# Optimization experiments

Measured on AMD Instinct MI355X. Metric: run time of the kernel, lower is better.

Reference implementation:

```python
import jax, jax.numpy as jnp
import numpy as np

B, S, HID = 2, 2048, 2048
H, KV, D = 16, 4, 128
THETA = 10000.0


def _apply_rope(x):
    # x: [B, h, S, D]; rotate even/odd interleaved halves, concat (original layout)
    seq = x.shape[2]
    pos = jnp.arange(seq, dtype=jnp.float32)
    inv_freq = 1.0 / (THETA ** (jnp.arange(0, D, 2, dtype=jnp.float32) / D))
    freqs = pos[:, None] * inv_freq[None, :]            # [S, D/2]
    cos = jnp.cos(freqs)[None, None]                    # [1,1,S,D/2]
    sin = jnp.sin(freqs)[None, None]
    x1, x2 = x[..., ::2], x[..., 1::2]
    return jnp.concatenate([x1 * cos - x2 * sin, x1 * sin + x2 * cos], axis=-1)


def setup_inputs() -> dict:
    key = jax.random.key(0)
    ks = jax.random.split(key, 5)
    x = jax.random.normal(ks[0], (B, S, HID), jnp.float32)
    Wq = jax.random.normal(ks[1], (HID, H * D), jnp.float32) * 0.02
    Wk = jax.random.normal(ks[2], (HID, KV * D), jnp.float32) * 0.02
    Wv = jax.random.normal(ks[3], (HID, KV * D), jnp.float32) * 0.02
    Wo = jax.random.normal(ks[4], (H * D, HID), jnp.float32) * 0.02
    mask = jnp.tril(jnp.ones((S, S), jnp.int32))[None, None]  # causal [1,1,S,S]
    return {"x": x, "mask": mask, "Wq": Wq, "Wk": Wk, "Wv": Wv, "Wo": Wo}


def reference(x, mask, Wq, Wk, Wv, Wo):
    b, s, _ = x.shape
    q = (x @ Wq).reshape(b, s, H, D).transpose(0, 2, 1, 3)   # [B,H,S,D]
    k = (x @ Wk).reshape(b, s, KV, D).transpose(0, 2, 1, 3)  # [B,KV,S,D]
    v = (x @ Wv).reshape(b, s, KV, D).transpose(0, 2, 1, 3)
    q = _apply_rope(q)
    k = _apply_rope(k)
    rep = H // KV
    k = jnp.repeat(k, rep, axis=1)  # GQA repeat_interleave -> [B,H,S,D]
    v = jnp.repeat(v, rep, axis=1)
    scores = jnp.einsum('bhqd,bhkd->bhqk', q, k) / jnp.sqrt(jnp.float32(D))
    scores = jnp.where(mask == 0, -jnp.inf, scores)
    attn = jax.nn.softmax(scores, axis=-1)  # dropout p=0 -> identity
    out = jnp.einsum('bhqk,bhkd->bhqd', attn, v)
    out = out.transpose(0, 2, 1, 3).reshape(b, s, H * D)
    return out @ Wo
```

## Files before the change

### kernel.cpp

```cpp
#include <hip/hip_runtime.h>
#include <cstdint>


typedef __attribute__((ext_vector_type(8))) short short8;
typedef __attribute__((ext_vector_type(8))) _Float16 half8;
typedef __attribute__((ext_vector_type(2))) __fp16 fp16x2;
typedef __attribute__((ext_vector_type(4))) float f32x4;
typedef __attribute__((ext_vector_type(16))) float f32x16;
typedef unsigned short u16;
typedef unsigned int u32;

#define NLOG_THETA_D2 (-0.14391156831212787f)
#define QSC_L2E 0.12751779437543f
#define M2SHIFT 17.3123404906676f

__device__ __forceinline__ u16 f2bf(float f) {
    u32 u = __float_as_uint(f);
    u += 0x7fffu + ((u >> 16) & 1u);
    return (u16)(u >> 16);
}
__device__ __forceinline__ float bf2f(u16 u) { return __uint_as_float(((u32)u) << 16); }
__device__ __forceinline__ u16 bf2h(u16 b) {
    union { _Float16 h; u16 u; } cv;
    cv.h = (_Float16)bf2f(b);
    return cv.u;
}
__device__ __forceinline__ u16 f2h(float f) {
    union { _Float16 h; u16 u; } cv;
    cv.h = (_Float16)f;
    return cv.u;
}
__device__ __forceinline__ float fast_exp2(float x) { return __builtin_amdgcn_exp2f(x); }

__device__ __forceinline__ void async_copy16(const void* g, void* lds) {
    __builtin_amdgcn_global_load_lds(
        (const __attribute__((address_space(1))) u32*)(uintptr_t)g,
        (__attribute__((address_space(3))) u32*)(uintptr_t)lds, 16, 0, 0);
}

__global__ __launch_bounds__(256)
void prep_kernel(const float* __restrict__ x, const float* __restrict__ Wq,
                 const float* __restrict__ Wk, const float* __restrict__ Wv,
                 u16* __restrict__ xb, u16* __restrict__ Wqkvt) {
    __shared__ float tile[32][33];
    int blk = blockIdx.x;
    if (blk < 8192) {
        int i = blk * 256 + threadIdx.x;
        float4 v = ((const float4*)x)[i];
        ushort4 o;
        o.x = f2bf(v.x); o.y = f2bf(v.y); o.z = f2bf(v.z); o.w = f2bf(v.w);
        ((ushort4*)xb)[i] = o;
        return;
    }
    const float* in; int C, orow, bx, by;
    if (blk < 12288)      { int j = blk - 8192;  in = Wq; C = 2048; orow = 0;    bx = j & 63; by = j >> 6; }
    else if (blk < 13312) { int j = blk - 12288; in = Wk; C = 512;  orow = 2048; bx = j & 15; by = j >> 4; }
    else                  { int j = blk - 13312; in = Wv; C = 512;  orow = 2560; bx = j & 15; by = j >> 4; }
    int r0 = by * 32, c0 = bx * 32;
    int tx = threadIdx.x & 31, ty = threadIdx.x >> 5;
#pragma unroll
    for (int j = 0; j < 4; ++j)
        tile[ty + j * 8][tx] = in[(size_t)(r0 + ty + j * 8) * C + c0 + tx];
    __syncthreads();
#pragma unroll
    for (int j = 0; j < 4; ++j)
        Wqkvt[(size_t)(orow + c0 + ty + j * 8) * 2048 + r0 + tx] = f2bf(tile[tx][ty + j * 8]);
}

__global__ __launch_bounds__(256)
void rope_vt_kernel(const u16* __restrict__ qkv, const float* __restrict__ Wo,
                    u16* __restrict__ qR, u16* __restrict__ kR,
                    u16* __restrict__ vT, u16* __restrict__ Wot) {
    int blk = blockIdx.x;
    if (blk < 4096) {
        int row = blk;
        float pos = (float)(row & 2047);
        const u16* rbase = qkv + (size_t)row * 3072;
        for (int t = threadIdx.x; t < 640; t += 256) {
            ushort4 uv; int c4; u16* ob; float sc;
            if (t < 512) {
                c4 = t * 4; uv = *(const ushort4*)(rbase + c4);
                ob = qR + (size_t)row * 2048 + (c4 & ~127); sc = QSC_L2E;
            } else {
                int u = t - 512; c4 = u * 4; uv = *(const ushort4*)(rbase + 2048 + c4);
                ob = kR + (size_t)row * 512 + (c4 & ~127); sc = 1.0f;
            }
            int j = (c4 & 127) >> 1;
            float x0 = bf2f(uv.x), x1 = bf2f(uv.y), x2 = bf2f(uv.z), x3 = bf2f(uv.w);
            float s1, c1, s2, c2;
            sincosf(pos * __expf(NLOG_THETA_D2 * (float)j), &s1, &c1);
            sincosf(pos * __expf(NLOG_THETA_D2 * (float)(j + 1)), &s2, &c2);
            float o1 = (x0 * c1 - x1 * s1) * sc;
            float o2 = (x2 * c2 - x3 * s2) * sc;
            float o3 = (x0 * s1 + x1 * c1) * sc;
            float o4 = (x2 * s2 + x3 * c2) * sc;
            *(u32*)&ob[j]      = (u32)f2bf(o1) | ((u32)f2bf(o2) << 16);
            *(u32*)&ob[64 + j] = (u32)f2bf(o3) | ((u32)f2bf(o4) << 16);
        }
        return;
    }
    int tx = threadIdx.x & 31, ty = threadIdx.x >> 5;
    if (blk < 6144) {
        __shared__ u16 tile[32][33];
        int j = blk - 4096;
        int b = j >> 10, rem = j & 1023;
        int c0 = (rem & 15) * 32, r0 = (rem >> 4) * 32;
        const u16* in = qkv + (size_t)b * 2048 * 3072 + 2560;
        u16* out = vT + (size_t)b * 512 * 2048;
#pragma unroll
        for (int i = 0; i < 4; ++i)
            tile[ty + i * 8][tx] = in[(size_t)(r0 + ty + i * 8) * 3072 + c0 + tx];
        __syncthreads();
#pragma unroll
        for (int i = 0; i < 4; ++i)
            out[(size_t)(c0 + ty + i * 8) * 2048 + r0 + tx] = bf2h(tile[tx][ty + i * 8]);
        return;
    }
    {
        __shared__ float tile[32][33];
        int j = blk - 6144;
        int c0 = (j & 63) * 32, r0 = (j >> 6) * 32;
#pragma unroll
        for (int i = 0; i < 4; ++i)
            tile[ty + i * 8][tx] = Wo[(size_t)(r0 + ty + i * 8) * 2048 + c0 + tx];
        __syncthreads();
#pragma unroll
        for (int i = 0; i < 4; ++i)
            Wot[(size_t)(c0 + ty + i * 8) * 2048 + r0 + tx] = f2bf(tile[tx][ty + i * 8]);
    }
}

template <int OBF>
__global__ __launch_bounds__(256)
void gemm_bf16(const u16* __restrict__ A, const u16* __restrict__ Bt,
               void* __restrict__ Cout, int M, int N, int K) {
    __shared__ __align__(16) u16 As[128 * 32];
    __shared__ __align__(16) u16 Bs[128 * 32];
    const int tid = threadIdx.x, wid = tid >> 6, lane = tid & 63;
    const int quad = lane >> 4, l16 = lane & 15;
    const int m0 = blockIdx.y * 128, n0 = blockIdx.x * 128;
    const int wm0 = (wid >> 1) * 64, wn0 = (wid & 1) * 64;
    f32x4 acc[4][4] = {};

    for (int k0 = 0; k0 < K; k0 += 32) {
#pragma unroll
        for (int rr = 0; rr < 2; ++rr) {
            int s = rr * 256 + wid * 64 + lane;
            int row = s >> 2;
            int c = (s & 3) ^ ((row >> 1) & 3);
            async_copy16(A + (size_t)(m0 + row) * K + k0 + c * 8,
                         &As[(size_t)(rr * 256 + wid * 64) * 8]);
            async_copy16(Bt + (size_t)(n0 + row) * K + k0 + c * 8,
                         &Bs[(size_t)(rr * 256 + wid * 64) * 8]);
        }
        __syncthreads();
        short8 a[4], b[4];
#pragma unroll
        for (int i = 0; i < 4; ++i) {
            int ra = wm0 + i * 16 + l16;
            a[i] = *(const short8*)&As[ra * 32 + ((quad ^ ((ra >> 1) & 3)) << 3)];
            int rb = wn0 + i * 16 + l16;
            b[i] = *(const short8*)&Bs[rb * 32 + ((quad ^ ((rb >> 1) & 3)) << 3)];
        }
#pragma unroll
        for (int i = 0; i < 4; ++i)
#pragma unroll
            for (int j = 0; j < 4; ++j)
                acc[i][j] = __builtin_amdgcn_mfma_f32_16x16x32_bf16(a[i], b[j], acc[i][j], 0, 0, 0);
        __syncthreads();
    }
#pragma unroll
    for (int i = 0; i < 4; ++i) {
        int rb = m0 + wm0 + i * 16 + quad * 4;
#pragma unroll
        for (int j = 0; j < 4; ++j) {
            int col = n0 + wn0 + j * 16 + l16;
#pragma unroll
            for (int r = 0; r < 4; ++r) {
                if (OBF) ((u16*)Cout)[(size_t)(rb + r) * N + col] = f2bf(acc[i][j][r]);
                else     ((float*)Cout)[(size_t)(rb + r) * N + col] = acc[i][j][r];
            }
        }
    }
}

__global__ __launch_bounds__(256, 2)
void attn_kernel(const u16* __restrict__ qR, const u16* __restrict__ kR,
                 const u16* __restrict__ vT, u16* __restrict__ ao,
                 u16* __restrict__ Opart, float* __restrict__ lpart) {
    __shared__ __align__(16) u16 bufK[2][64 * 128];
    __shared__ __align__(16) u16 bufV[2][128 * 64];
    const int tid = threadIdx.x, wid = tid >> 6, lane = tid & 63;
    const int l31 = lane & 31, h = lane >> 5;
    const int b = blockIdx.z, hh = blockIdx.y;
    const int bx = blockIdx.x;
    int qt, t0, nt, chunk;
    bool split;
    if (bx < 16) {
        qt = 15 - (bx >> 1); chunk = bx & 1; split = true;
        nt = qt + 1; t0 = chunk ? (qt + 1) : 0;
    } else {
        qt = 23 - bx; chunk = 0; split = false;
        nt = 2 * qt + 2; t0 = 0;
    }
    const int kvh = hh >> 2;
    const int q0 = qt * 128;
    const u16* kB = kR + (size_t)b * 2048 * 512 + kvh * 128;
    const u16* vB = vT + (size_t)(b * 512 + kvh * 128) * 2048;

    const u16* kSrc[4]; const u16* vSrc[4]; int ldsOff[4];
#pragma unroll
    for (int rr = 0; rr < 4; ++rr) {
        int s = rr * 256 + wid * 64 + lane;
        int rK = s >> 4, cK = (s & 15) ^ (rK & 7);
        kSrc[rr] = kB + (size_t)(t0 * 64 + rK) * 512 + cK * 8;
        int rV = s >> 3, cV = (s & 7) ^ (rV & 7);
        vSrc[rr] = vB + (size_t)rV * 2048 + t0 * 64 + cV * 8;
        ldsOff[rr] = (rr * 256 + wid * 64) * 8;
    }
    auto stage = [&](int buf) {
#pragma unroll
        for (int rr = 0; rr < 4; ++rr) {
            async_copy16(kSrc[rr], &bufK[buf][ldsOff[rr]]);
            async_copy16(vSrc[rr], &bufV[buf][ldsOff[rr]]);
            kSrc[rr] += 64 * 512;
            vSrc[rr] += 64;
        }
    };

    const int rq = wid * 32 + l31;
    const u16* qrow = qR + (size_t)(b * 2048 + q0 + rq) * 2048 + hh * 128;
    short8 aQ[8];
#pragma unroll
    for (int kd = 0; kd < 8; ++kd)
        aQ[kd] = *(const short8*)(qrow + kd * 16 + h * 8);

    f32x16 oacc[4] = {};
    float lp = 0.f;
    const int qg = q0 + rq;

    stage(0);
    for (int t = 0; t < nt; ++t) {
        const int cur = t & 1;
        __syncthreads();
        if (t + 1 < nt) stage(cur ^ 1);

        f32x16 sacc[2] = {};
#pragma unroll
        for (int kd = 0; kd < 8; ++kd)
#pragma unroll
            for (int mt = 0; mt < 2; ++mt) {
                int rk = mt * 32 + l31;
                short8 aK = *(const short8*)&bufK[cur][rk * 128 + (((kd * 2 + h) ^ (rk & 7)) << 3)];
                sacc[mt] = __builtin_amdgcn_mfma_f32_32x32x16_bf16(aK, aQ[kd], sacc[mt], 0, 0, 0);
            }

        const int tg = t0 + t;
        const int kk0 = tg * 64;
        u32 pk[2][8];
        const bool domask = (tg >= 2 * qt);
        auto softpack = [&](bool dm) {
#pragma unroll
            for (int mt = 0; mt < 2; ++mt) {
                const int kvb = kk0 + mt * 32 + 4 * h;
#pragma unroll
                for (int p = 0; p < 8; ++p) {
                    int r0 = 2 * p;
                    float s0 = sacc[mt][r0], s1 = sacc[mt][r0 + 1];
                    float p0, p1;
                    if (dm) {
                        int kv0 = kvb + (r0 & 3) + 8 * (r0 >> 2);
                        p0 = (kv0 <= qg)     ? fast_exp2(s0 - M2SHIFT) : 0.f;
                        p1 = (kv0 + 1 <= qg) ? fast_exp2(s1 - M2SHIFT) : 0.f;
                    } else {
                        p0 = fast_exp2(s0 - M2SHIFT);
                        p1 = fast_exp2(s1 - M2SHIFT);
                    }
                    lp += p0 + p1;
                    union { fp16x2 h; u32 u; } cv;
                    cv.h = __builtin_amdgcn_cvt_pkrtz(p0, p1);
                    pk[mt][p] = cv.u;
                }
            }
        };
        if (domask) softpack(true); else softpack(false);

#pragma unroll
        for (int ks = 0; ks < 4; ++ks) {
            int mt = ks >> 1, k2 = ks & 1;
            u32 own0 = pk[mt][4 * k2 + 2 * h + 0];
            u32 own1 = pk[mt][4 * k2 + 2 * h + 1];
            u32 snd0 = pk[mt][4 * k2 + 2 * (h ^ 1) + 0];
            u32 snd1 = pk[mt][4 * k2 + 2 * (h ^ 1) + 1];
            u32 rc0 = __shfl_xor((int)snd0, 32, 64);
            u32 rc1 = __shfl_xor((int)snd1, 32, 64);
            union { half8 v; u32 u[4]; } bP;
            bP.u[0] = h ? rc0 : own0;
            bP.u[1] = h ? rc1 : own1;
            bP.u[2] = h ? own0 : rc0;
            bP.u[3] = h ? own1 : rc1;
#pragma unroll
            for (int dt = 0; dt < 4; ++dt) {
                int rv = dt * 32 + l31;
                union { short8 s; half8 v; } aV;
                aV.s = *(const short8*)&bufV[cur][rv * 64 + (((ks * 2 + h) ^ (rv & 7)) << 3)];
                oacc[dt] = __builtin_amdgcn_mfma_f32_32x32x16_f16(aV.v, bP.v, oacc[dt], 0, 0, 0);
            }
        }
    }

    lp += __shfl_xor(lp, 32, 64);

    if (!split) {
        float linv = 1.0f / lp;
        u16* orow = ao + (size_t)(b * 2048 + qg) * 2048 + hh * 128;
#pragma unroll
        for (int dt = 0; dt < 4; ++dt)
#pragma unroll
            for (int g = 0; g < 4; ++g) {
                ushort4 o4;
                o4.x = f2bf(oacc[dt][4 * g + 0] * linv);
                o4.y = f2bf(oacc[dt][4 * g + 1] * linv);
                o4.z = f2bf(oacc[dt][4 * g + 2] * linv);
                o4.w = f2bf(oacc[dt][4 * g + 3] * linv);
                *(ushort4*)&orow[dt * 32 + 8 * g + 4 * h] = o4;
            }
    } else {
        const int gi = ((b * 16 + hh) * 8 + (qt - 8)) * 2 + chunk;
        u16* prow = Opart + ((size_t)gi * 128 + rq) * 128;
#pragma unroll
        for (int dt = 0; dt < 4; ++dt)
#pragma unroll
            for (int g = 0; g < 4; ++g) {
                ushort4 o4;
                o4.x = f2h(oacc[dt][4 * g + 0]);
                o4.y = f2h(oacc[dt][4 * g + 1]);
                o4.z = f2h(oacc[dt][4 * g + 2]);
                o4.w = f2h(oacc[dt][4 * g + 3]);
                *(ushort4*)&prow[dt * 32 + 8 * g + 4 * h] = o4;
            }
        if (h == 0) lpart[gi * 128 + rq] = lp;
    }
}

__global__ __launch_bounds__(256)
void combine_kernel(const u16* __restrict__ Opart, const float* __restrict__ lpart,
                    u16* __restrict__ ao) {
    const int gi = blockIdx.x;
    const int q8 = gi & 7, hh = (gi >> 3) & 15, b = gi >> 7;
    const int r = threadIdx.x >> 1, hf = threadIdx.x & 1;
    const size_t p0 = (((size_t)gi * 2 + 0) * 128 + r) * 128 + hf * 64;
    const size_t p1 = (((size_t)gi * 2 + 1) * 128 + r) * 128 + hf * 64;
    const float l0 = lpart[(gi * 2 + 0) * 128 + r];
    const float l1 = lpart[(gi * 2 + 1) * 128 + r];
    const float inv = 1.0f / (l0 + l1);
    u16* orow = ao + ((size_t)(b * 2048 + (q8 + 8) * 128 + r)) * 2048 + hh * 128 + hf * 64;
#pragma unroll
    for (int c = 0; c < 8; ++c) {
        half8 a = *(const half8*)&Opart[p0 + c * 8];
        half8 d = *(const half8*)&Opart[p1 + c * 8];
        union { ushort4 q[2]; u16 e[8]; } o;
#pragma unroll
        for (int j = 0; j < 8; ++j)
            o.e[j] = f2bf(((float)a[j] + (float)d[j]) * inv);
        *(ushort4*)&orow[c * 8]     = o.q[0];
        *(ushort4*)&orow[c * 8 + 4] = o.q[1];
    }
}

extern "C" void kernel_launch(void* const* d_in, const int* in_sizes, int n_in,
                              void* d_out, int out_size, void* d_ws, size_t ws_size,
                              hipStream_t stream) {
    const float* x  = (const float*)d_in[0];
    const float* Wq = (const float*)d_in[2];
    const float* Wk = (const float*)d_in[3];
    const float* Wv = (const float*)d_in[4];
    const float* Wo = (const float*)d_in[5];
    float* out = (float*)d_out;

    char* ws = (char*)d_ws;
    u16* Wqkvt = (u16*)(ws);
    u16* Wot   = Wqkvt;
    u16* xb_ao = (u16*)(ws + 12582912);
    u16* qkv   = (u16*)(ws + 29360128);
    u16* Opart = (u16*)(ws + 29360128);
    float* lpart = (float*)(ws + 29360128 + 16777216);
    u16* qR    = (u16*)(ws + 54525952);
    u16* kR    = (u16*)(ws + 71303168);
    u16* vT    = (u16*)(ws + 75497472);

    dim3 blk(256);
    prep_kernel<<<14336, blk, 0, stream>>>(x, Wq, Wk, Wv, xb_ao, Wqkvt);
    gemm_bf16<1><<<dim3(24, 32), blk, 0, stream>>>(xb_ao, Wqkvt, qkv, 4096, 3072, 2048);
    rope_vt_kernel<<<10240, blk, 0, stream>>>(qkv, Wo, qR, kR, vT, Wot);
    attn_kernel<<<dim3(24, 16, 2), blk, 0, stream>>>(qR, kR, vT, xb_ao, Opart, lpart);
    combine_kernel<<<256, blk, 0, stream>>>(Opart, lpart, xb_ao);
    gemm_bf16<0><<<dim3(16, 32), blk, 0, stream>>>(xb_ao, Wot, out, 4096, 2048, 2048);
}
```

Before: 388.0 us.

## Load K/V directly from global in attention, drop LDS staging, XCD-aware block mapping

The attention kernel stops staging K and V tiles through double-buffered shared memory with async copies and barriers. Each lane now reads its MFMA operands straight from global memory (relying on L2 for reuse across the four waves and the GQA head group). A 1D grid is remapped so that blocks sharing a batch and KV head land on the same XCD, and launch bounds are raised to allow 4 blocks per CU. This removes LDS traffic and syncs, but every wave now issues redundant global loads with no prefetch overlap, so memory latency may be exposed.

```diff
diff --git a/kernel.cpp b/kernel.cpp
--- a/kernel.cpp
+++ b/kernel.cpp
@@ -184,49 +184,37 @@
     }
 }
 
-__global__ __launch_bounds__(256, 2)
+__global__ __launch_bounds__(256, 4)
 void attn_kernel(const u16* __restrict__ qR, const u16* __restrict__ kR,
                  const u16* __restrict__ vT, u16* __restrict__ ao,
                  u16* __restrict__ Opart, float* __restrict__ lpart) {
-    __shared__ __align__(16) u16 bufK[2][64 * 128];
-    __shared__ __align__(16) u16 bufV[2][128 * 64];
     const int tid = threadIdx.x, wid = tid >> 6, lane = tid & 63;
     const int l31 = lane & 31, h = lane >> 5;
-    const int b = blockIdx.z, hh = blockIdx.y;
-    const int bx = blockIdx.x;
+    const int bid = blockIdx.x;
+    const int xcd = bid & 7;
+    const int b = xcd >> 2, kvh = xcd & 3;
+    const int j = bid >> 3;
+    const int hh = kvh * 4 + (j & 3);
+    const int sched = j >> 2;
     int qt, t0, nt, chunk;
     bool split;
-    if (bx < 16) {
-        qt = 15 - (bx >> 1); chunk = bx & 1; split = true;
+    if (sched < 16) {
+        qt = 15 - (sched >> 1); chunk = sched & 1; split = true;
         nt = qt + 1; t0 = chunk ? (qt + 1) : 0;
     } else {
-        qt = 23 - bx; chunk = 0; split = false;
+        qt = 23 - sched; chunk = 0; split = false;
         nt = 2 * qt + 2; t0 = 0;
     }
-    const int kvh = hh >> 2;
     const int q0 = qt * 128;
     const u16* kB = kR + (size_t)b * 2048 * 512 + kvh * 128;
     const u16* vB = vT + (size_t)(b * 512 + kvh * 128) * 2048;
 
-    const u16* kSrc[4]; const u16* vSrc[4]; int ldsOff[4];
-#pragma unroll
-    for (int rr = 0; rr < 4; ++rr) {
-        int s = rr * 256 + wid * 64 + lane;
-        int rK = s >> 4, cK = (s & 15) ^ (rK & 7);
-        kSrc[rr] = kB + (size_t)(t0 * 64 + rK) * 512 + cK * 8;
-        int rV = s >> 3, cV = (s & 7) ^ (rV & 7);
-        vSrc[rr] = vB + (size_t)rV * 2048 + t0 * 64 + cV * 8;
-        ldsOff[rr] = (rr * 256 + wid * 64) * 8;
-    }
-    auto stage = [&](int buf) {
-#pragma unroll
-        for (int rr = 0; rr < 4; ++rr) {
-            async_copy16(kSrc[rr], &bufK[buf][ldsOff[rr]]);
-            async_copy16(vSrc[rr], &bufV[buf][ldsOff[rr]]);
-            kSrc[rr] += 64 * 512;
-            vSrc[rr] += 64;
-        }
-    };
+    const u16* kP0 = kB + (size_t)(t0 * 64 + l31) * 512 + h * 8;
+    const u16* kP1 = kP0 + (size_t)32 * 512;
+    const u16* vP0 = vB + (size_t)l31 * 2048 + t0 * 64 + h * 8;
+    const u16* vP1 = vP0 + (size_t)32 * 2048;
+    const u16* vP2 = vP0 + (size_t)64 * 2048;
+    const u16* vP3 = vP0 + (size_t)96 * 2048;
 
     const int rq = wid * 32 + l31;
     const u16* qrow = qR + (size_t)(b * 2048 + q0 + rq) * 2048 + hh * 128;
@@ -239,21 +227,16 @@
     float lp = 0.f;
     const int qg = q0 + rq;
 
-    stage(0);
     for (int t = 0; t < nt; ++t) {
-        const int cur = t & 1;
-        __syncthreads();
-        if (t + 1 < nt) stage(cur ^ 1);
-
         f32x16 sacc[2] = {};
 #pragma unroll
-        for (int kd = 0; kd < 8; ++kd)
-#pragma unroll
-            for (int mt = 0; mt < 2; ++mt) {
-                int rk = mt * 32 + l31;
-                short8 aK = *(const short8*)&bufK[cur][rk * 128 + (((kd * 2 + h) ^ (rk & 7)) << 3)];
-                sacc[mt] = __builtin_amdgcn_mfma_f32_32x32x16_bf16(aK, aQ[kd], sacc[mt], 0, 0, 0);
-            }
+        for (int kd = 0; kd < 8; ++kd) {
+            sacc[0] = __builtin_amdgcn_mfma_f32_32x32x16_bf16(
+                *(const short8*)(kP0 + kd * 16), aQ[kd], sacc[0], 0, 0, 0);
+            sacc[1] = __builtin_amdgcn_mfma_f32_32x32x16_bf16(
+                *(const short8*)(kP1 + kd * 16), aQ[kd], sacc[1], 0, 0, 0);
+        }
+        kP0 += 64 * 512; kP1 += 64 * 512;
 
         const int tg = t0 + t;
         const int kk0 = tg * 64;
@@ -299,14 +282,17 @@
             bP.u[1] = h ? rc1 : own1;
             bP.u[2] = h ? own0 : rc0;
             bP.u[3] = h ? own1 : rc1;
-#pragma unroll
-            for (int dt = 0; dt < 4; ++dt) {
-                int rv = dt * 32 + l31;
-                union { short8 s; half8 v; } aV;
-                aV.s = *(const short8*)&bufV[cur][rv * 64 + (((ks * 2 + h) ^ (rv & 7)) << 3)];
-                oacc[dt] = __builtin_amdgcn_mfma_f32_32x32x16_f16(aV.v, bP.v, oacc[dt], 0, 0, 0);
-            }
-        }
+            union { short8 s; half8 v; } aV0, aV1, aV2, aV3;
+            aV0.s = *(const short8*)(vP0 + ks * 16);
+            aV1.s = *(const short8*)(vP1 + ks * 16);
+            aV2.s = *(const short8*)(vP2 + ks * 16);
+            aV3.s = *(const short8*)(vP3 + ks * 16);
+            oacc[0] = __builtin_amdgcn_mfma_f32_32x32x16_f16(aV0.v, bP.v, oacc[0], 0, 0, 0);
+            oacc[1] = __builtin_amdgcn_mfma_f32_32x32x16_f16(aV1.v, bP.v, oacc[1], 0, 0, 0);
+            oacc[2] = __builtin_amdgcn_mfma_f32_32x32x16_f16(aV2.v, bP.v, oacc[2], 0, 0, 0);
+            oacc[3] = __builtin_amdgcn_mfma_f32_32x32x16_f16(aV3.v, bP.v, oacc[3], 0, 0, 0);
+        }
+        vP0 += 64; vP1 += 64; vP2 += 64; vP3 += 64;
     }
 
     lp += __shfl_xor(lp, 32, 64);
@@ -393,7 +379,7 @@
     prep_kernel<<<14336, blk, 0, stream>>>(x, Wq, Wk, Wv, xb_ao, Wqkvt);
     gemm_bf16<1><<<dim3(24, 32), blk, 0, stream>>>(xb_ao, Wqkvt, qkv, 4096, 3072, 2048);
     rope_vt_kernel<<<10240, blk, 0, stream>>>(qkv, Wo, qR, kR, vT, Wot);
-    attn_kernel<<<dim3(24, 16, 2), blk, 0, stream>>>(qR, kR, vT, xb_ao, Opart, lpart);
+    attn_kernel<<<768, blk, 0, stream>>>(qR, kR, vT, xb_ao, Opart, lpart);
     combine_kernel<<<256, blk, 0, stream>>>(Opart, lpart, xb_ao);
     gemm_bf16<0><<<dim3(16, 32), blk, 0, stream>>>(xb_ao, Wot, out, 4096, 2048, 2048);
 }
```

Result: slower. 511.0 us (+31.7%).

## Share K/V tiles across two GQA heads per 512-thread attention block

Applied to the files above, without the earlier changes.

The attention kernel now runs 512 threads per block, and the two groups of four waves each handle a different query head that maps to the same KV head. Each K/V tile loaded into LDS is therefore reused by two heads, halving K/V global traffic and staging work per head. The grid is flattened to 384 blocks, with the group index in the low bits so the longest query tiles are scheduled first. In exchange, larger blocks with launch_bounds(512,2) may raise register pressure and reduce how flexibly blocks can be scheduled.

```diff
diff --git a/kernel.cpp b/kernel.cpp
--- a/kernel.cpp
+++ b/kernel.cpp
@@ -184,7 +184,7 @@
     }
 }
 
-__global__ __launch_bounds__(256, 2)
+__global__ __launch_bounds__(512, 2)
 void attn_kernel(const u16* __restrict__ qR, const u16* __restrict__ kR,
                  const u16* __restrict__ vT, u16* __restrict__ ao,
                  u16* __restrict__ Opart, float* __restrict__ lpart) {
@@ -192,35 +192,38 @@
     __shared__ __align__(16) u16 bufV[2][128 * 64];
     const int tid = threadIdx.x, wid = tid >> 6, lane = tid & 63;
     const int l31 = lane & 31, h = lane >> 5;
-    const int b = blockIdx.z, hh = blockIdx.y;
-    const int bx = blockIdx.x;
+    const int bid = blockIdx.x;
+    const int g = bid & 15;
+    const int b = g >> 3, kvh = (g >> 1) & 3, hp = g & 1;
+    const int hw = kvh * 4 + hp * 2 + (wid >> 2);
+    const int wq = wid & 3;
+    const int sched = bid >> 4;
     int qt, t0, nt, chunk;
     bool split;
-    if (bx < 16) {
-        qt = 15 - (bx >> 1); chunk = bx & 1; split = true;
+    if (sched < 16) {
+        qt = 15 - (sched >> 1); chunk = sched & 1; split = true;
         nt = qt + 1; t0 = chunk ? (qt + 1) : 0;
     } else {
-        qt = 23 - bx; chunk = 0; split = false;
+        qt = 23 - sched; chunk = 0; split = false;
         nt = 2 * qt + 2; t0 = 0;
     }
-    const int kvh = hh >> 2;
     const int q0 = qt * 128;
     const u16* kB = kR + (size_t)b * 2048 * 512 + kvh * 128;
     const u16* vB = vT + (size_t)(b * 512 + kvh * 128) * 2048;
 
-    const u16* kSrc[4]; const u16* vSrc[4]; int ldsOff[4];
-#pragma unroll
-    for (int rr = 0; rr < 4; ++rr) {
-        int s = rr * 256 + wid * 64 + lane;
+    const u16* kSrc[2]; const u16* vSrc[2]; int ldsOff[2];
+#pragma unroll
+    for (int rr = 0; rr < 2; ++rr) {
+        int s = rr * 512 + tid;
         int rK = s >> 4, cK = (s & 15) ^ (rK & 7);
         kSrc[rr] = kB + (size_t)(t0 * 64 + rK) * 512 + cK * 8;
         int rV = s >> 3, cV = (s & 7) ^ (rV & 7);
         vSrc[rr] = vB + (size_t)rV * 2048 + t0 * 64 + cV * 8;
-        ldsOff[rr] = (rr * 256 + wid * 64) * 8;
+        ldsOff[rr] = (rr * 512 + wid * 64) * 8;
     }
     auto stage = [&](int buf) {
 #pragma unroll
-        for (int rr = 0; rr < 4; ++rr) {
+        for (int rr = 0; rr < 2; ++rr) {
             async_copy16(kSrc[rr], &bufK[buf][ldsOff[rr]]);
             async_copy16(vSrc[rr], &bufV[buf][ldsOff[rr]]);
             kSrc[rr] += 64 * 512;
@@ -228,8 +231,8 @@
         }
     };
 
-    const int rq = wid * 32 + l31;
-    const u16* qrow = qR + (size_t)(b * 2048 + q0 + rq) * 2048 + hh * 128;
+    const int rq = wq * 32 + l31;
+    const u16* qrow = qR + (size_t)(b * 2048 + q0 + rq) * 2048 + hw * 128;
     short8 aQ[8];
 #pragma unroll
     for (int kd = 0; kd < 8; ++kd)
@@ -313,31 +316,31 @@
 
     if (!split) {
         float linv = 1.0f / lp;
-        u16* orow = ao + (size_t)(b * 2048 + qg) * 2048 + hh * 128;
+        u16* orow = ao + (size_t)(b * 2048 + qg) * 2048 + hw * 128;
 #pragma unroll
         for (int dt = 0; dt < 4; ++dt)
 #pragma unroll
-            for (int g = 0; g < 4; ++g) {
+            for (int gg = 0; gg < 4; ++gg) {
                 ushort4 o4;
-                o4.x = f2bf(oacc[dt][4 * g + 0] * linv);
-                o4.y = f2bf(oacc[dt][4 * g + 1] * linv);
-                o4.z = f2bf(oacc[dt][4 * g + 2] * linv);
-                o4.w = f2bf(oacc[dt][4 * g + 3] * linv);
-                *(ushort4*)&orow[dt * 32 + 8 * g + 4 * h] = o4;
+                o4.x = f2bf(oacc[dt][4 * gg + 0] * linv);
+                o4.y = f2bf(oacc[dt][4 * gg + 1] * linv);
+                o4.z = f2bf(oacc[dt][4 * gg + 2] * linv);
+                o4.w = f2bf(oacc[dt][4 * gg + 3] * linv);
+                *(ushort4*)&orow[dt * 32 + 8 * gg + 4 * h] = o4;
             }
     } else {
-        const int gi = ((b * 16 + hh) * 8 + (qt - 8)) * 2 + chunk;
+        const int gi = ((b * 16 + hw) * 8 + (qt - 8)) * 2 + chunk;
         u16* prow = Opart + ((size_t)gi * 128 + rq) * 128;
 #pragma unroll
         for (int dt = 0; dt < 4; ++dt)
 #pragma unroll
-            for (int g = 0; g < 4; ++g) {
+            for (int gg = 0; gg < 4; ++gg) {
                 ushort4 o4;
-                o4.x = f2h(oacc[dt][4 * g + 0]);
-                o4.y = f2h(oacc[dt][4 * g + 1]);
-                o4.z = f2h(oacc[dt][4 * g + 2]);
-                o4.w = f2h(oacc[dt][4 * g + 3]);
-                *(ushort4*)&prow[dt * 32 + 8 * g + 4 * h] = o4;
+                o4.x = f2h(oacc[dt][4 * gg + 0]);
+                o4.y = f2h(oacc[dt][4 * gg + 1]);
+                o4.z = f2h(oacc[dt][4 * gg + 2]);
+                o4.w = f2h(oacc[dt][4 * gg + 3]);
+                *(ushort4*)&prow[dt * 32 + 8 * gg + 4 * h] = o4;
             }
         if (h == 0) lpart[gi * 128 + rq] = lp;
     }
@@ -393,7 +396,7 @@
     prep_kernel<<<14336, blk, 0, stream>>>(x, Wq, Wk, Wv, xb_ao, Wqkvt);
     gemm_bf16<1><<<dim3(24, 32), blk, 0, stream>>>(xb_ao, Wqkvt, qkv, 4096, 3072, 2048);
     rope_vt_kernel<<<10240, blk, 0, stream>>>(qkv, Wo, qR, kR, vT, Wot);
-    attn_kernel<<<dim3(24, 16, 2), blk, 0, stream>>>(qR, kR, vT, xb_ao, Opart, lpart);
+    attn_kernel<<<384, dim3(512), 0, stream>>>(qR, kR, vT, xb_ao, Opart, lpart);
     combine_kernel<<<256, blk, 0, stream>>>(Opart, lpart, xb_ao);
     gemm_bf16<0><<<dim3(16, 32), blk, 0, stream>>>(xb_ao, Wot, out, 4096, 2048, 2048);
 }
```

Measured after the change: 375.9 us. 1.03x faster.
